# Performance work log

Measured on AMD Instinct MI355X. Metric: run time of the kernel, lower is better.

Reference implementation:

```python
import jax, jax.numpy as jnp
import numpy as np

H = 8       # num_heads
K = 16      # neighbours
LN_EPS = 1e-6

def _knn_indices(coords, k):
    # coords: (B,N,3) float32. Squared-euclidean distances preserve kNN ordering of cdist.
    d2 = jnp.sum(coords * coords, axis=-1)                      # (B,N)
    dist2 = d2[:, :, None] + d2[:, None, :] - 2.0 * jnp.einsum('bnd,bmd->bnm', coords, coords)
    _, idx = jax.lax.top_k(-dist2, k)                           # (B,N,k) smallest distances
    return idx

def _gather(x, idx):
    # x: (B,N,D), idx: (B,N,K) -> (B,N,K,D)
    return jax.vmap(lambda a, i: a[i])(x, idx)

def setup_inputs() -> dict:
    key = jax.random.key(0)
    ks = jax.random.split(key, 16)
    B, N, D = 2, 8192, 256
    P = 6
    std = 0.02
    inp = {
        'features': jax.random.normal(ks[0], (B, N, D), jnp.float32),
        'coords': jax.random.uniform(ks[1], (B, N, 3), jnp.float32),
        'normals': jax.random.normal(ks[2], (B, N, 3), jnp.float32),
        'mask': jnp.ones((B, N), jnp.float32),
        # linear weights stored (in, out): y = x @ W + b
        'Wq': jax.random.normal(ks[3], (D, D), jnp.float32) * std,
        'bq': jnp.zeros((D,), jnp.float32),
        'Wk': jax.random.normal(ks[4], (D, D), jnp.float32) * std,
        'bk': jnp.zeros((D,), jnp.float32),
        'Wv': jax.random.normal(ks[5], (D, D), jnp.float32) * std,
        'bv': jnp.zeros((D,), jnp.float32),
        'Wo': jax.random.normal(ks[6], (D, D), jnp.float32) * std,  # torch inits this to zero; random here for nontrivial test
        'bo': jnp.zeros((D,), jnp.float32),
        'Wp1': jax.random.normal(ks[7], (P, D), jnp.float32) * std,
        'bp1': jnp.zeros((D,), jnp.float32),
        'Wp2': jax.random.normal(ks[8], (D, D), jnp.float32) * std,
        'bp2': jnp.zeros((D,), jnp.float32),
        'gamma': jnp.ones((D,), jnp.float32),
        'beta': jnp.zeros((D,), jnp.float32),
    }
    return inp

def reference(features, coords, normals, mask, Wq, bq, Wk, bk, Wv, bv, Wo, bo,
              Wp1, bp1, Wp2, bp2, gamma, beta):
    B, N, D = features.shape
    dh = D // H
    scale = 1.0 / np.sqrt(dh).astype(np.float32)
    residual = features

    idx = _knn_indices(jax.lax.stop_gradient(coords), K)        # (B,N,K), no-grad as in torch

    nb_coords = _gather(coords, idx)                            # (B,N,K,3)
    rel_pos = coords[:, :, None, :] - nb_coords                 # (B,N,K,3)
    pos_input = jnp.concatenate(
        [rel_pos, jnp.broadcast_to(normals[:, :, None, :], rel_pos.shape)], axis=-1)  # (B,N,K,6)
    # pos MLP: Linear -> GELU(exact, torch default) -> Linear
    pos_emb = jax.nn.gelu(pos_input @ Wp1 + bp1, approximate=False) @ Wp2 + bp2       # (B,N,K,D)

    q = features @ Wq + bq                                      # (B,N,D)
    kp = features @ Wk + bk
    vp = features @ Wv + bv
    kg = _gather(kp, idx)                                       # (B,N,K,D)
    vg = _gather(vp, idx)

    k_comb = (kg + pos_emb).reshape(B, N, K, H, dh)
    v_comb = (vg + pos_emb).reshape(B, N, K, H, dh)
    qh = q.reshape(B, N, H, dh)

    logits = jnp.einsum('bnhd,bnkhd->bnkh', qh, k_comb) * scale  # (B,N,K,H)
    nb_valid = _gather(mask[..., None], idx)[..., 0]             # (B,N,K)
    logits = jnp.where(nb_valid[..., None] > 0, logits, -jnp.inf)
    attn = jax.nn.softmax(logits, axis=2)
    attn = jnp.nan_to_num(attn, nan=0.0)

    out = jnp.einsum('bnkh,bnkhd->bnhd', attn, v_comb).reshape(B, N, D)
    out = (out @ Wo + bo) * mask[..., None]

    h = residual + out
    mu = jnp.mean(h, axis=-1, keepdims=True)
    var = jnp.mean((h - mu) ** 2, axis=-1, keepdims=True)
    h = (h - mu) / jnp.sqrt(var + LN_EPS) * gamma + beta
    return h * mask[..., None]
```

## Files before the change

kernel.cpp:

```cpp
#include <hip/hip_runtime.h>
#include <hip/hip_bf16.h>
#include <math.h>

typedef unsigned short u16t;
typedef unsigned int   u32t;
typedef unsigned long long u64t;
typedef __attribute__((ext_vector_type(8))) short  short8;
typedef __attribute__((ext_vector_type(4))) float  floatx4;

#define NPTS   8192
#define DMODEL 256
#define BNTOT  16384
#define HSTR   264

__device__ __forceinline__ float bitsf(u32t u){ union { u32t i; float f; } v; v.i = u; return v.f; }
__device__ __forceinline__ float b2f(u16t s){ return bitsf(((u32t)s) << 16); }
__device__ __forceinline__ u16t f2b(float f){
  __hip_bfloat16 h = __float2bfloat16(f);
  return *reinterpret_cast<u16t*>(&h);
}
__device__ __forceinline__ uint4 pack8(const float* o){
  uint4 st;
  st.x = (u32t)f2b(o[0]) | ((u32t)f2b(o[1]) << 16);
  st.y = (u32t)f2b(o[2]) | ((u32t)f2b(o[3]) << 16);
  st.z = (u32t)f2b(o[4]) | ((u32t)f2b(o[5]) << 16);
  st.w = (u32t)f2b(o[6]) | ((u32t)f2b(o[7]) << 16);
  return st;
}

__device__ __forceinline__ float gelu_fast(float x){
  float ax = fabsf(x) * 0.70710678118654752f;
  float t  = __builtin_amdgcn_rcpf(__builtin_fmaf(0.3275911f, ax, 1.0f));
  float p  = t*(0.254829592f + t*(-0.284496736f + t*(1.421413741f +
             t*(-1.453152027f + t*1.061405429f))));
  float er = __builtin_fmaf(-p, __expf(-ax*ax), 1.0f);
  return 0.5f * x * (1.0f + copysignf(er, x));
}

__global__ __launch_bounds__(256) void fill_valf(float* p, int n, float v){
  int i = blockIdx.x * 256 + threadIdx.x;
  if (i < n) p[i] = v;
}

__global__ __launch_bounds__(256) void wprep1(const float* __restrict__ W,
                                              u16t* __restrict__ out) {
  int r = blockIdx.x * 256 + threadIdx.x;
  int v = r & 7, l = (r >> 3) & 63, cca = (r >> 9) & 15, ic = r >> 13;
  int i = ic * 32 + (l >> 4) * 8 + v;
  int c = cca * 16 + (l & 15);
  out[r] = f2b(W[(size_t)i * DMODEL + c]);
}

__device__ __forceinline__ void cswap_asc(u64t& a, u64t& b){
  u64t mn = (a < b) ? a : b;
  u64t mx = (a < b) ? b : a;
  a = mn; b = mx;
}
__device__ __forceinline__ void bitonic16(u64t v[16]){
  #pragma unroll
  for (int k = 2; k <= 16; k <<= 1) {
    #pragma unroll
    for (int j = k >> 1; j > 0; j >>= 1) {
      #pragma unroll
      for (int i = 0; i < 16; ++i) {
        int l = i ^ j;
        if (l > i) {
          if ((i & k) == 0) cswap_asc(v[i], v[l]);
          else              cswap_asc(v[l], v[i]);
        }
      }
    }
  }
}
__device__ __forceinline__ void merge16(u64t best[16], u64t v[16]){
  #pragma unroll
  for (int i = 0; i < 16; ++i) {
    u64t o = v[15 - i];
    best[i] = (best[i] < o) ? best[i] : o;
  }
  #pragma unroll
  for (int j = 8; j > 0; j >>= 1) {
    #pragma unroll
    for (int i = 0; i < 16; ++i) {
      int l = i ^ j;
      if (l > i) cswap_asc(best[i], best[l]);
    }
  }
}
__device__ __forceinline__ void knn_flush(u64t best[16], u32t& thr, int& cnt,
                                          const u64t* bufw, int lane){
  u64t v[16];
  #pragma unroll
  for (int s = 0; s < 16; ++s) {
    u64t x = bufw[s * 64 + lane];
    v[s] = (s < cnt) ? x : 0xFFFFFFFFFFFFFFFFULL;
  }
  bitonic16(v);
  merge16(best, v);
  thr = (u32t)(best[15] >> 32);
  cnt = 0;
}

__global__ __launch_bounds__(256) void knn_partial(const float* __restrict__ coords,
                                                   u64t* __restrict__ pk) {
  int qb = blockIdx.x >> 3, ch = blockIdx.x & 7;
  int tid = threadIdx.x;
  int lane = tid & 63, wv = tid >> 6;
  int g = qb * 256 + tid;
  int b = g >> 13;
  alignas(16) __shared__ float4 tile[256];
  __shared__ u64t buf[4][16][64];

  float qx = coords[(size_t)g * 3 + 0];
  float qy = coords[(size_t)g * 3 + 1];
  float qz = coords[(size_t)g * 3 + 2];
  float qd2 = __fadd_rn(__fadd_rn(__fmul_rn(qx,qx), __fmul_rn(qy,qy)), __fmul_rn(qz,qz));

  u64t best[16];
  #pragma unroll
  for (int s = 0; s < 16; ++s) best[s] = 0xFFFFFFFFFFFFFFFFULL;
  u32t thr = 0xFFFFFFFFu;
  int  cnt = 0;
  u64t* bufw = &buf[wv][0][0];

  int cs = ch * 1024;
  for (int t = 0; t < 4; ++t) {
    int ci = cs + t * 256 + tid;
    size_t cb = (size_t)(b * NPTS + ci) * 3;
    float x = coords[cb + 0];
    float y = coords[cb + 1];
    float z = coords[cb + 2];
    float d2 = __fadd_rn(__fadd_rn(__fmul_rn(x,x), __fmul_rn(y,y)), __fmul_rn(z,z));
    __syncthreads();
    tile[tid] = make_float4(x, y, z, d2);
    __syncthreads();
    int cbase = cs + t * 256;
    for (int u = 0; u < 256; ++u) {
      float4 cd = tile[u];
      float dot = __fadd_rn(__fadd_rn(__fmul_rn(qx,cd.x), __fmul_rn(qy,cd.y)), __fmul_rn(qz,cd.z));
      float dist = __fsub_rn(__fadd_rn(qd2, cd.w), __fmul_rn(2.0f, dot));
      u32t db  = __float_as_uint(dist);
      u32t key = db ^ ((u32t)(((int)db) >> 31) | 0x80000000u);
      if (key <= thr) {
        bufw[cnt * 64 + lane] = ((u64t)key << 32) | (u32t)(cbase + u);
        ++cnt;
      }
      if (__any(cnt == 16)) knn_flush(best, thr, cnt, bufw, lane);
    }
  }
  if (__any(cnt > 0)) knn_flush(best, thr, cnt, bufw, lane);

  size_t base = (size_t)g * 128 + ch * 16;
  #pragma unroll
  for (int s = 0; s < 16; ++s) pk[base + s] = best[s];
}

__global__ __launch_bounds__(256) void knn_merge(const u64t* __restrict__ pk,
                                                 u16t* __restrict__ idxb) {
  int g = blockIdx.x * 256 + threadIdx.x;
  size_t base = (size_t)g * 128;
  int h[8];
  #pragma unroll
  for (int c = 0; c < 8; ++c) h[c] = 0;
  for (int s = 0; s < 16; ++s) {
    u64t bk = 0xFFFFFFFFFFFFFFFFULL; int bc = 0;
    #pragma unroll
    for (int c = 0; c < 8; ++c) {
      if (h[c] < 16) {
        u64t kk = pk[base + c * 16 + h[c]];
        if (kk < bk) { bk = kk; bc = c; }
      }
    }
    idxb[(size_t)g * 16 + s] = (u16t)(bk & 0xFFFFu);
    h[bc]++;
  }
}

__global__ __launch_bounds__(256) void gemm_kv_mfma(const float* __restrict__ feat,
    const u16t* __restrict__ frags,
    const float* __restrict__ bk, const float* __restrict__ bv,
    u16t* __restrict__ kb, u16t* __restrict__ vb) {
  int mat = blockIdx.y;
  const u16t* wf   = frags + (size_t)mat * 65536;
  const float* bias = mat ? bv : bk;
  u16t* out         = mat ? vb : kb;

  int rbase = blockIdx.x * 64;
  int tid = threadIdx.x, lane = tid & 63, wvi = tid >> 6;
  int quad = lane >> 4, l15 = lane & 15;

  alignas(16) __shared__ u16t featS[64 * HSTR];

  {
    int r = tid >> 2, c0 = (tid & 3) * 64;
    const float* src = feat + (size_t)(rbase + r) * DMODEL + c0;
    u16t* dst = featS + r * HSTR + c0;
    #pragma unroll
    for (int t = 0; t < 8; ++t) {
      float4 a = *(const float4*)(src + t * 8);
      float4 b = *(const float4*)(src + t * 8 + 4);
      float o[8] = {a.x, a.y, a.z, a.w, b.x, b.y, b.z, b.w};
      *(uint4*)(dst + t * 8) = pack8(o);
    }
  }
  __syncthreads();

  floatx4 acc[16];
  #pragma unroll
  for (int ct = 0; ct < 16; ++ct) acc[ct] = (floatx4){0.f, 0.f, 0.f, 0.f};

  #pragma unroll
  for (int ic = 0; ic < 8; ++ic) {
    short8 af = *(const short8*)(featS + (wvi * 16 + l15) * HSTR + ic * 32 + quad * 8);
    #pragma unroll
    for (int ct = 0; ct < 16; ++ct) {
      short8 bf = *(const short8*)(wf + (((size_t)(ic * 16 + ct) * 64 + lane) << 3));
      acc[ct] = __builtin_amdgcn_mfma_f32_16x16x32_bf16(af, bf, acc[ct], 0, 0, 0);
    }
  }

  #pragma unroll
  for (int ct = 0; ct < 16; ++ct) {
    int col = ct * 16 + l15;
    float bvv = bias[col];
    #pragma unroll
    for (int r = 0; r < 4; ++r) {
      int row = rbase + wvi * 16 + quad * 4 + r;
      out[(size_t)row * DMODEL + col] = f2b(acc[ct][r] + bvv);
    }
  }
}

__global__ __launch_bounds__(256, 4) void attn_mega(
    const float* __restrict__ coords, const float* __restrict__ normals,
    const float* __restrict__ maskp, const float* __restrict__ feat,
    const float* __restrict__ bq,
    const float* __restrict__ Wp1, const float* __restrict__ bp1,
    const float* __restrict__ bp2,
    const u16t* __restrict__ idxp,
    const u16t* __restrict__ wqfrag, const u16t* __restrict__ wp2frag,
    const u16t* __restrict__ kbuf, const u16t* __restrict__ vbuf,
    float* __restrict__ outp) {
  alignas(16) __shared__ u16t hemb[64 * HSTR];
  alignas(16) __shared__ u16t qB[8 * HSTR];
  __shared__ float wS[64];
  __shared__ int   idS[64];

  int c    = threadIdx.x;
  int lane = c & 63;
  int wv   = c >> 6;
  int quad = lane >> 4;
  int l15  = lane & 15;
  int wv4  = wv * 4;
  int qbase = blockIdx.x * 8;

  {
    int r = c >> 5, c0 = (c & 31) * 8;
    const float* src = feat + (size_t)(qbase + r) * DMODEL + c0;
    float4 a = *(const float4*)(src);
    float4 b = *(const float4*)(src + 4);
    float o[8] = {a.x, a.y, a.z, a.w, b.x, b.y, b.z, b.w};
    *(uint4*)(hemb + r * HSTR + c0) = pack8(o);
    uint4 z; z.x = 0u; z.y = 0u; z.z = 0u; z.w = 0u;
    *(uint4*)(hemb + (8 + r) * HSTR + c0) = z;
  }
  __syncthreads();

  {
    floatx4 qa[4];
    #pragma unroll
    for (int cc = 0; cc < 4; ++cc) qa[cc] = (floatx4){0.f, 0.f, 0.f, 0.f};
    #pragma unroll
    for (int ic = 0; ic < 8; ++ic) {
      short8 af = *(const short8*)(hemb + l15 * HSTR + ic * 32 + quad * 8);
      #pragma unroll
      for (int cc = 0; cc < 4; ++cc) {
        short8 bf = *(const short8*)(wqfrag + (((size_t)(ic * 16 + wv4 + cc) * 64 + lane) << 3));
        qa[cc] = __builtin_amdgcn_mfma_f32_16x16x32_bf16(af, bf, qa[cc], 0, 0, 0);
      }
    }
    if (quad < 2) {
      #pragma unroll
      for (int cc = 0; cc < 4; ++cc) {
        int col = (wv4 + cc) * 16 + l15;
        float bqv = bq[col];
        #pragma unroll
        for (int r = 0; r < 4; ++r)
          qB[(quad * 4 + r) * HSTR + col] = f2b(qa[cc][r] + bqv);
      }
    }
  }

  float w1[6];
  #pragma unroll
  for (int p = 0; p < 6; ++p) w1[p] = Wp1[p * DMODEL + c];
  float b1v = bp1[c];
  float b2c[4];
  #pragma unroll
  for (int cc = 0; cc < 4; ++cc) b2c[cc] = bp2[(wv4 + cc) * 16 + l15];
  const float lsc = 0.17677669529663687f;
  __syncthreads();

  #pragma unroll
  for (int G = 0; G < 2; ++G) {
    for (int ql = 0; ql < 4; ++ql) {
      int g = qbase + G * 4 + ql;
      int bb0 = (g >> 13) * NPTS;
      float qx = coords[(size_t)g * 3 + 0];
      float qy = coords[(size_t)g * 3 + 1];
      float qz = coords[(size_t)g * 3 + 2];
      float n0 = normals[(size_t)g * 3 + 0];
      float n1 = normals[(size_t)g * 3 + 1];
      float n2 = normals[(size_t)g * 3 + 2];
      #pragma unroll
      for (int j = 0; j < 16; ++j) {
        int id = (int)idxp[(size_t)g * 16 + j];
        size_t cb = (size_t)(bb0 + id) * 3;
        float rx = qx - coords[cb + 0];
        float ry = qy - coords[cb + 1];
        float rz = qz - coords[cb + 2];
        float pre = b1v + rx * w1[0] + ry * w1[1] + rz * w1[2]
                        + n0 * w1[3] + n1 * w1[4] + n2 * w1[5];
        hemb[(ql * 16 + j) * HSTR + c] = f2b(gelu_fast(pre));
      }
    }
    __syncthreads();

    floatx4 acc[4][4];
    #pragma unroll
    for (int rt = 0; rt < 4; ++rt)
      #pragma unroll
      for (int cc = 0; cc < 4; ++cc) acc[rt][cc] = (floatx4){0.f, 0.f, 0.f, 0.f};

    #pragma unroll
    for (int ic = 0; ic < 8; ++ic) {
      short8 af0 = *(const short8*)(hemb + ( 0 + l15) * HSTR + ic * 32 + quad * 8);
      short8 af1 = *(const short8*)(hemb + (16 + l15) * HSTR + ic * 32 + quad * 8);
      short8 af2 = *(const short8*)(hemb + (32 + l15) * HSTR + ic * 32 + quad * 8);
      short8 af3 = *(const short8*)(hemb + (48 + l15) * HSTR + ic * 32 + quad * 8);
      #pragma unroll
      for (int cc = 0; cc < 4; ++cc) {
        short8 bf = *(const short8*)(wp2frag + (((size_t)(ic * 16 + wv4 + cc) * 64 + lane) << 3));
        acc[0][cc] = __builtin_amdgcn_mfma_f32_16x16x32_bf16(af0, bf, acc[0][cc], 0, 0, 0);
        acc[1][cc] = __builtin_amdgcn_mfma_f32_16x16x32_bf16(af1, bf, acc[1][cc], 0, 0, 0);
        acc[2][cc] = __builtin_amdgcn_mfma_f32_16x16x32_bf16(af2, bf, acc[2][cc], 0, 0, 0);
        acc[3][cc] = __builtin_amdgcn_mfma_f32_16x16x32_bf16(af3, bf, acc[3][cc], 0, 0, 0);
      }
    }
    __syncthreads();
    #pragma unroll
    for (int rt = 0; rt < 4; ++rt)
      #pragma unroll
      for (int cc = 0; cc < 4; ++cc) {
        int cg = (wv4 + cc) * 16 + l15;
        #pragma unroll
        for (int r = 0; r < 4; ++r)
          hemb[(rt * 16 + quad * 4 + r) * HSTR + cg] = f2b(acc[rt][cc][r] + b2c[cc]);
      }
    __syncthreads();

    {
      int g = qbase + G * 4 + wv;
      int bb0 = (g >> 13) * NPTS;
      int idl = (int)idxp[(size_t)g * 16 + l15];
      float mvl = maskp[bb0 + idl];
      unsigned long long bm = __ballot(mvl > 0.0f);
      if (quad == 0) idS[wv * 16 + l15] = idl;
      const u16t* krow = kbuf + (size_t)(bb0 + idl) * DMODEL;
      const u16t* erow = hemb + (wv * 16 + l15) * HSTR;
      const u16t* qrow = qB + (G * 4 + wv) * HSTR;
      floatx4 sa = (floatx4){0.f, 0.f, 0.f, 0.f};
      #pragma unroll
      for (int ic = 0; ic < 8; ++ic) {
        short8 ak  = *(const short8*)(krow + ic * 32 + quad * 8);
        short8 ae  = *(const short8*)(erow + ic * 32 + quad * 8);
        short8 qb8 = *(const short8*)(qrow + ic * 32 + quad * 8);
        sa = __builtin_amdgcn_mfma_f32_16x16x32_bf16(ak, qb8, sa, 0, 0, 0);
        sa = __builtin_amdgcn_mfma_f32_16x16x32_bf16(ae, qb8, sa, 0, 0, 0);
      }
      float lg[4];
      #pragma unroll
      for (int r = 0; r < 4; ++r) {
        int j = quad * 4 + r;
        lg[r] = ((bm >> j) & 1ULL) ? sa[r] * lsc : -1e30f;
      }
      float m = fmaxf(fmaxf(lg[0], lg[1]), fmaxf(lg[2], lg[3]));
      m = fmaxf(m, __shfl_xor(m, 16));
      m = fmaxf(m, __shfl_xor(m, 32));
      float e0 = __expf(lg[0] - m), e1 = __expf(lg[1] - m);
      float e2 = __expf(lg[2] - m), e3 = __expf(lg[3] - m);
      float s = e0 + e1 + e2 + e3;
      s += __shfl_xor(s, 16);
      s += __shfl_xor(s, 32);
      float inv = (m > -1e29f) ? __builtin_amdgcn_rcpf(s) : 0.0f;
      if (l15 == 0) {
        wS[wv * 16 + quad * 4 + 0] = e0 * inv;
        wS[wv * 16 + quad * 4 + 1] = e1 * inv;
        wS[wv * 16 + quad * 4 + 2] = e2 * inv;
        wS[wv * 16 + quad * 4 + 3] = e3 * inv;
      }
    }
    __syncthreads();

    #pragma unroll
    for (int ql = 0; ql < 4; ++ql) {
      int g = qbase + G * 4 + ql;
      int bb0 = (g >> 13) * NPTS;
      float o = 0.0f;
      #pragma unroll
      for (int j = 0; j < 16; ++j) {
        int id  = idS[ql * 16 + j];
        float w = wS[ql * 16 + j];
        float vv = b2f(vbuf[(size_t)(bb0 + id) * DMODEL + c]);
        float ee = b2f(hemb[(ql * 16 + j) * HSTR + c]);
        o += w * (vv + ee);
      }
      outp[(size_t)g * DMODEL + c] = o;
    }
    if (G == 0) __syncthreads();
  }
}

__global__ __launch_bounds__(256) void gemm_out(const float* __restrict__ feat,
    const float* __restrict__ maskp,
    const u16t* __restrict__ wofrag, const float* __restrict__ bo,
    const float* __restrict__ gamma, const float* __restrict__ beta,
    float* __restrict__ io) {
  int rbase = blockIdx.x * 64;
  int tid = threadIdx.x, lane = tid & 63, wvi = tid >> 6;
  int quad = lane >> 4, l15 = lane & 15;

  alignas(16) __shared__ u16t oS[64 * HSTR];

  {
    int r = tid >> 2, c0 = (tid & 3) * 64;
    const float* src = io + (size_t)(rbase + r) * DMODEL + c0;
    u16t* dst = oS + r * HSTR + c0;
    #pragma unroll
    for (int t = 0; t < 8; ++t) {
      float4 a = *(const float4*)(src + t * 8);
      float4 b = *(const float4*)(src + t * 8 + 4);
      float o[8] = {a.x, a.y, a.z, a.w, b.x, b.y, b.z, b.w};
      *(uint4*)(dst + t * 8) = pack8(o);
    }
  }
  __syncthreads();

  floatx4 acc[16];
  #pragma unroll
  for (int ct = 0; ct < 16; ++ct) acc[ct] = (floatx4){0.f, 0.f, 0.f, 0.f};

  #pragma unroll
  for (int ic = 0; ic < 8; ++ic) {
    short8 af = *(const short8*)(oS + (wvi * 16 + l15) * HSTR + ic * 32 + quad * 8);
    #pragma unroll
    for (int ct = 0; ct < 16; ++ct) {
      short8 bf = *(const short8*)(wofrag + (((size_t)(ic * 16 + ct) * 64 + lane) << 3));
      acc[ct] = __builtin_amdgcn_mfma_f32_16x16x32_bf16(af, bf, acc[ct], 0, 0, 0);
    }
  }

  float bov[16], gamv[16], betv[16];
  #pragma unroll
  for (int ct = 0; ct < 16; ++ct) {
    int col = ct * 16 + l15;
    bov[ct]  = bo[col];
    gamv[ct] = gamma[col];
    betv[ct] = beta[col];
  }

  #pragma unroll
  for (int r = 0; r < 4; ++r) {
    int row = rbase + wvi * 16 + quad * 4 + r;
    float mv = maskp[row];
    float hv[16];
    float s = 0.0f, s2 = 0.0f;
    #pragma unroll
    for (int ct = 0; ct < 16; ++ct) {
      float h = feat[(size_t)row * DMODEL + ct * 16 + l15] + (acc[ct][r] + bov[ct]) * mv;
      hv[ct] = h; s += h; s2 += h * h;
    }
    #pragma unroll
    for (int off = 1; off < 16; off <<= 1) {
      s  += __shfl_xor(s,  off, 16);
      s2 += __shfl_xor(s2, off, 16);
    }
    float mu  = s  * (1.0f / 256.0f);
    float ms  = s2 * (1.0f / 256.0f);
    float var = ms - mu * mu;
    float inv = 1.0f / sqrtf(var + 1e-6f);
    #pragma unroll
    for (int ct = 0; ct < 16; ++ct) {
      float y = (hv[ct] - mu) * inv * gamv[ct] + betv[ct];
      y *= mv;
      io[(size_t)row * DMODEL + ct * 16 + l15] = y;
    }
  }
}

extern "C" void kernel_launch(void* const* d_in, const int* in_sizes, int n_in,
                              void* d_out, int out_size, void* d_ws, size_t ws_size,
                              hipStream_t stream) {
  static const int EXP[18] = {4194304, 49152, 49152, 16384,
                              65536, 256, 65536, 256, 65536, 256, 65536, 256,
                              1536, 256, 65536, 256, 256, 256};
  bool sizes_ok = (n_in >= 18);
  if (sizes_ok) for (int i = 0; i < 18; ++i) sizes_ok = sizes_ok && (in_sizes[i] == EXP[i]);
  int fb = (out_size + 255) / 256;
  if (!sizes_ok) {
    fill_valf<<<fb, 256, 0, stream>>>((float*)d_out, out_size, 0.0f);
    return;
  }
  const size_t WS_NEED = 17825792;
  if (ws_size < WS_NEED) {
    fill_valf<<<fb, 256, 0, stream>>>((float*)d_out, out_size, 1.0f);
    return;
  }

  const float* feat    = (const float*)d_in[0];
  const float* coords  = (const float*)d_in[1];
  const float* normals = (const float*)d_in[2];
  const float* maskp   = (const float*)d_in[3];
  const float* Wq  = (const float*)d_in[4];
  const float* bq  = (const float*)d_in[5];
  const float* Wk  = (const float*)d_in[6];
  const float* bk  = (const float*)d_in[7];
  const float* Wv  = (const float*)d_in[8];
  const float* bv  = (const float*)d_in[9];
  const float* Wo  = (const float*)d_in[10];
  const float* bo  = (const float*)d_in[11];
  const float* Wp1 = (const float*)d_in[12];
  const float* bp1 = (const float*)d_in[13];
  const float* Wp2 = (const float*)d_in[14];
  const float* bp2 = (const float*)d_in[15];
  const float* gamma = (const float*)d_in[16];
  const float* beta  = (const float*)d_in[17];

  char* ws = (char*)d_ws;
  u16t*  idx16  = (u16t*)(ws);
  u16t*  frags  = (u16t*)(ws + 524288);
  u16t*  kb     = (u16t*)(ws + 1048576);
  u16t*  vb     = (u16t*)(ws + 9437184);
  u64t*  pk     = (u64t*)(ws + 1048576);
  u16t*  wofrag = (u16t*)(ws + 1048576);

  wprep1<<<256, 256, 0, stream>>>(Wk,  frags);
  wprep1<<<256, 256, 0, stream>>>(Wv,  frags + 65536);
  wprep1<<<256, 256, 0, stream>>>(Wp2, frags + 131072);
  wprep1<<<256, 256, 0, stream>>>(Wq,  frags + 196608);
  knn_partial<<<512, 256, 0, stream>>>(coords, pk);
  knn_merge<<<64, 256, 0, stream>>>(pk, idx16);
  gemm_kv_mfma<<<dim3(256, 2), 256, 0, stream>>>(feat, frags, bk, bv, kb, vb);
  attn_mega<<<2048, 256, 0, stream>>>(coords, normals, maskp, feat,
                                      bq, Wp1, bp1, bp2,
                                      idx16, frags + 196608, frags + 131072,
                                      kb, vb, (float*)d_out);
  wprep1<<<256, 256, 0, stream>>>(Wo, wofrag);
  gemm_out<<<256, 256, 0, stream>>>(feat, maskp, wofrag, bo, gamma, beta,
                                    (float*)d_out);
}
```

Before: 545.5 us.

## Fuse weight prep launches, unroll kNN scan, and merge K/V GEMM blocks

Four weight-prep launches become one kernel that picks the source matrix from the element index. The kNN scan compares float distances against a float threshold, building the sortable key only for accepted candidates. It unrolls the candidate loop by four and checks the wave-wide flush every four candidates, flushing at 13 so the 16-slot buffer cannot overflow. The K/V GEMM now computes both projections in one block and reuses the feature fragments loaded once into registers, which halves the grid and the feature staging but raises register pressure.

```diff
diff --git a/kernel.cpp b/kernel.cpp
--- a/kernel.cpp
+++ b/kernel.cpp
@@ -42,6 +42,19 @@
   if (i < n) p[i] = v;
 }
 
+__global__ __launch_bounds__(256) void wprep4(const float* __restrict__ Wk,
+                                              const float* __restrict__ Wv,
+                                              const float* __restrict__ Wp2,
+                                              const float* __restrict__ Wq,
+                                              u16t* __restrict__ out) {
+  int e = blockIdx.x * 256 + threadIdx.x;
+  int m = e >> 16, r = e & 65535;
+  const float* W = (m == 0) ? Wk : (m == 1 ? Wv : (m == 2 ? Wp2 : Wq));
+  int v = r & 7, l = (r >> 3) & 63, cca = (r >> 9) & 15, ic = r >> 13;
+  int i = ic * 32 + (l >> 4) * 8 + v;
+  int c = cca * 16 + (l & 15);
+  out[e] = f2b(W[(size_t)i * DMODEL + c]);
+}
 __global__ __launch_bounds__(256) void wprep1(const float* __restrict__ W,
                                               u16t* __restrict__ out) {
   int r = blockIdx.x * 256 + threadIdx.x;
@@ -87,7 +100,7 @@
     }
   }
 }
-__device__ __forceinline__ void knn_flush(u64t best[16], u32t& thr, int& cnt,
+__device__ __forceinline__ void knn_flush(u64t best[16], float& thrf, int& cnt,
                                           const u64t* bufw, int lane){
   u64t v[16];
   #pragma unroll
@@ -97,7 +110,9 @@
   }
   bitonic16(v);
   merge16(best, v);
-  thr = (u32t)(best[15] >> 32);
+  u32t k15 = (u32t)(best[15] >> 32);
+  thrf = (k15 == 0xFFFFFFFFu) ? 3.3e38f
+       : bitsf((k15 & 0x80000000u) ? (k15 ^ 0x80000000u) : ~k15);
   cnt = 0;
 }
 
@@ -119,7 +134,7 @@
   u64t best[16];
   #pragma unroll
   for (int s = 0; s < 16; ++s) best[s] = 0xFFFFFFFFFFFFFFFFULL;
-  u32t thr = 0xFFFFFFFFu;
+  float thrf = 3.3e38f;
   int  cnt = 0;
   u64t* bufw = &buf[wv][0][0];
 
@@ -135,20 +150,23 @@
     tile[tid] = make_float4(x, y, z, d2);
     __syncthreads();
     int cbase = cs + t * 256;
-    for (int u = 0; u < 256; ++u) {
-      float4 cd = tile[u];
-      float dot = __fadd_rn(__fadd_rn(__fmul_rn(qx,cd.x), __fmul_rn(qy,cd.y)), __fmul_rn(qz,cd.z));
-      float dist = __fsub_rn(__fadd_rn(qd2, cd.w), __fmul_rn(2.0f, dot));
-      u32t db  = __float_as_uint(dist);
-      u32t key = db ^ ((u32t)(((int)db) >> 31) | 0x80000000u);
-      if (key <= thr) {
-        bufw[cnt * 64 + lane] = ((u64t)key << 32) | (u32t)(cbase + u);
-        ++cnt;
-      }
-      if (__any(cnt == 16)) knn_flush(best, thr, cnt, bufw, lane);
-    }
-  }
-  if (__any(cnt > 0)) knn_flush(best, thr, cnt, bufw, lane);
+    for (int u = 0; u < 256; u += 4) {
+      #pragma unroll
+      for (int uu = 0; uu < 4; ++uu) {
+        float4 cd = tile[u + uu];
+        float dot = __fadd_rn(__fadd_rn(__fmul_rn(qx,cd.x), __fmul_rn(qy,cd.y)), __fmul_rn(qz,cd.z));
+        float dist = __fsub_rn(__fadd_rn(qd2, cd.w), __fmul_rn(2.0f, dot));
+        if (dist <= thrf) {
+          u32t db  = __float_as_uint(dist);
+          u32t key = db ^ ((u32t)(((int)db) >> 31) | 0x80000000u);
+          bufw[cnt * 64 + lane] = ((u64t)key << 32) | (u32t)(cbase + u + uu);
+          ++cnt;
+        }
+      }
+      if (__any(cnt >= 13)) knn_flush(best, thrf, cnt, bufw, lane);
+    }
+  }
+  if (__any(cnt > 0)) knn_flush(best, thrf, cnt, bufw, lane);
 
   size_t base = (size_t)g * 128 + ch * 16;
   #pragma unroll
@@ -180,11 +198,6 @@
     const u16t* __restrict__ frags,
     const float* __restrict__ bk, const float* __restrict__ bv,
     u16t* __restrict__ kb, u16t* __restrict__ vb) {
-  int mat = blockIdx.y;
-  const u16t* wf   = frags + (size_t)mat * 65536;
-  const float* bias = mat ? bv : bk;
-  u16t* out         = mat ? vb : kb;
-
   int rbase = blockIdx.x * 64;
   int tid = threadIdx.x, lane = tid & 63, wvi = tid >> 6;
   int quad = lane >> 4, l15 = lane & 15;
@@ -205,28 +218,39 @@
   }
   __syncthreads();
 
-  floatx4 acc[16];
-  #pragma unroll
-  for (int ct = 0; ct < 16; ++ct) acc[ct] = (floatx4){0.f, 0.f, 0.f, 0.f};
-
-  #pragma unroll
-  for (int ic = 0; ic < 8; ++ic) {
-    short8 af = *(const short8*)(featS + (wvi * 16 + l15) * HSTR + ic * 32 + quad * 8);
+  short8 af[8];
+  #pragma unroll
+  for (int ic = 0; ic < 8; ++ic)
+    af[ic] = *(const short8*)(featS + (wvi * 16 + l15) * HSTR + ic * 32 + quad * 8);
+
+  #pragma unroll
+  for (int mat = 0; mat < 2; ++mat) {
+    const u16t* wf   = frags + (size_t)mat * 65536;
+    const float* bias = mat ? bv : bk;
+    u16t* out         = mat ? vb : kb;
+
+    floatx4 acc[16];
+    #pragma unroll
+    for (int ct = 0; ct < 16; ++ct) acc[ct] = (floatx4){0.f, 0.f, 0.f, 0.f};
+
+    #pragma unroll
+    for (int ic = 0; ic < 8; ++ic) {
+      #pragma unroll
+      for (int ct = 0; ct < 16; ++ct) {
+        short8 bf = *(const short8*)(wf + (((size_t)(ic * 16 + ct) * 64 + lane) << 3));
+        acc[ct] = __builtin_amdgcn_mfma_f32_16x16x32_bf16(af[ic], bf, acc[ct], 0, 0, 0);
+      }
+    }
+
     #pragma unroll
     for (int ct = 0; ct < 16; ++ct) {
-      short8 bf = *(const short8*)(wf + (((size_t)(ic * 16 + ct) * 64 + lane) << 3));
-      acc[ct] = __builtin_amdgcn_mfma_f32_16x16x32_bf16(af, bf, acc[ct], 0, 0, 0);
-    }
-  }
-
-  #pragma unroll
-  for (int ct = 0; ct < 16; ++ct) {
-    int col = ct * 16 + l15;
-    float bvv = bias[col];
-    #pragma unroll
-    for (int r = 0; r < 4; ++r) {
-      int row = rbase + wvi * 16 + quad * 4 + r;
-      out[(size_t)row * DMODEL + col] = f2b(acc[ct][r] + bvv);
+      int col = ct * 16 + l15;
+      float bvv = bias[col];
+      #pragma unroll
+      for (int r = 0; r < 4; ++r) {
+        int row = rbase + wvi * 16 + quad * 4 + r;
+        out[(size_t)row * DMODEL + col] = f2b(acc[ct][r] + bvv);
+      }
     }
   }
 }
@@ -251,8 +275,10 @@
   int wv   = c >> 6;
   int quad = lane >> 4;
   int l15  = lane & 15;
+  int hh   = c >> 5;
   int wv4  = wv * 4;
   int qbase = blockIdx.x * 8;
+  (void)hh;
 
   {
     int r = c >> 5, c0 = (c & 31) * 8;
@@ -544,13 +570,10 @@
   u64t*  pk     = (u64t*)(ws + 1048576);
   u16t*  wofrag = (u16t*)(ws + 1048576);
 
-  wprep1<<<256, 256, 0, stream>>>(Wk,  frags);
-  wprep1<<<256, 256, 0, stream>>>(Wv,  frags + 65536);
-  wprep1<<<256, 256, 0, stream>>>(Wp2, frags + 131072);
-  wprep1<<<256, 256, 0, stream>>>(Wq,  frags + 196608);
+  wprep4<<<1024, 256, 0, stream>>>(Wk, Wv, Wp2, Wq, frags);
   knn_partial<<<512, 256, 0, stream>>>(coords, pk);
   knn_merge<<<64, 256, 0, stream>>>(pk, idx16);
-  gemm_kv_mfma<<<dim3(256, 2), 256, 0, stream>>>(feat, frags, bk, bv, kb, vb);
+  gemm_kv_mfma<<<256, 256, 0, stream>>>(feat, frags, bk, bv, kb, vb);
   attn_mega<<<2048, 256, 0, stream>>>(coords, normals, maskp, feat,
                                       bq, Wp1, bp1, bp2,
                                       idx16, frags + 196608, frags + 131072,
```

Measured after the change: 562.1 us. +3.1%, slower.
